# Performance work log

Hardware: AMD Instinct MI355X
Metric: run time of the kernel (lower is better)

The kernel has to match this reference:

```python
import jax, jax.numpy as jnp
import numpy as np

N_NODES = 50000
N_EDGES = 800000
D_IN = 128
D_OUT = 128


def setup_inputs() -> dict:
    key = jax.random.key(0)
    k1, k2, k3, k4, k5, k6 = jax.random.split(key, 6)
    x = jax.random.normal(k1, (N_NODES, D_IN), dtype=jnp.float32)
    edge_row = jax.random.randint(k2, (N_EDGES,), 0, N_NODES, dtype=jnp.int32)
    edge_col = jax.random.randint(k3, (N_EDGES,), 0, N_NODES, dtype=jnp.int32)
    edge_weight = jax.random.uniform(k4, (N_EDGES,), dtype=jnp.float32)
    W = jax.random.normal(k5, (D_OUT, D_IN), dtype=jnp.float32) * (1.0 / np.sqrt(D_IN))
    b = jax.random.normal(k6, (D_OUT,), dtype=jnp.float32) * 0.01
    return {"x": x, "edge_row": edge_row, "edge_col": edge_col,
            "edge_weight": edge_weight, "W": W, "b": b}


def reference(x, edge_row, edge_col, edge_weight, W, b):
    # SpMM: out[i] = sum_{e: row[e]==i} weight[e] * x[col[e]]
    msgs = edge_weight[:, None] * x[edge_col]            # [E, D_IN]
    agg = jax.ops.segment_sum(msgs, edge_row, num_segments=N_NODES)  # [N, D_IN]
    # nn.Linear: agg @ W.T + b
    return agg @ W.T + b
```

## Files before the change

### kernel.cpp

```cpp
#include <hip/hip_runtime.h>

#define D 128
#define PB 128
#define CAP 48

typedef __attribute__((ext_vector_type(8))) short bf16x8;
typedef __attribute__((ext_vector_type(4))) float f32x4;

__device__ __forceinline__ short f2bf_rne(float f) {
  unsigned u = __float_as_uint(f);
  unsigned r = u + 0x7fffu + ((u >> 16) & 1u);
  return (short)(r >> 16);
}

__device__ __forceinline__ bf16x8 pack_bf16x8(float4 a, float4 b) {
  bf16x8 h;
  h[0] = f2bf_rne(a.x); h[1] = f2bf_rne(a.y);
  h[2] = f2bf_rne(a.z); h[3] = f2bf_rne(a.w);
  h[4] = f2bf_rne(b.x); h[5] = f2bf_rne(b.y);
  h[6] = f2bf_rne(b.z); h[7] = f2bf_rne(b.w);
  return h;
}

__global__ __launch_bounds__(256) void part_gemm_kernel(
    const int* __restrict__ erow, const int* __restrict__ ecol,
    const float* __restrict__ ew, int* __restrict__ ncur,
    int2* __restrict__ swcol,
    const float* __restrict__ x, const float* __restrict__ W,
    ushort* __restrict__ y, int E, int N) {
  if (blockIdx.x < PB) {
    const int tid = threadIdx.x;
    const int chunk = (E + PB - 1) / PB;
    const int begin = blockIdx.x * chunk;
    const int end = min(begin + chunk, E);
    for (int e = begin + tid; e < end; e += 256) {
      int r = erow[e];
      int pos = atomicAdd(&ncur[r], 1);
      if (pos < CAP)
        swcol[(size_t)r * CAP + pos] =
            make_int2(ecol[e], __float_as_int(ew[e]));
    }
  } else {
    const int tid = threadIdx.x;
    const int wave = tid >> 6, lane = tid & 63;
    const int m_half = wave & 1;
    const int n_half = wave >> 1;
    const int l16 = lane & 15, quad = lane >> 4;

    bf16x8 Bf[4][4];
    const float4* W4 = (const float4*)W;
#pragma unroll
    for (int nt = 0; nt < 4; ++nt) {
      int n = n_half * 64 + nt * 16 + l16;
#pragma unroll
      for (int kb = 0; kb < 4; ++kb) {
        int idx = (n * D + kb * 32 + quad * 8) >> 2;
        Bf[nt][kb] = pack_bf16x8(W4[idx], W4[idx + 1]);
      }
    }

    const float4* x4 = (const float4*)x;
    const int ntiles = (N + 63) >> 6;
    const int gstride = gridDim.x - PB;
    for (int tile = (int)blockIdx.x - PB; tile < ntiles; tile += gstride) {
      const int row0 = tile * 64 + m_half * 32;
      f32x4 acc[2][4];
#pragma unroll
      for (int mt = 0; mt < 2; ++mt)
#pragma unroll
        for (int nt = 0; nt < 4; ++nt)
          acc[mt][nt] = (f32x4){0.f, 0.f, 0.f, 0.f};

#pragma unroll
      for (int kb = 0; kb < 4; ++kb) {
        const int k0 = kb * 32 + quad * 8;
        int m0 = row0 + l16;      if (m0 > N - 1) m0 = N - 1;
        int m1 = row0 + 16 + l16; if (m1 > N - 1) m1 = N - 1;
        int i0 = (m0 * D + k0) >> 2;
        int i1 = (m1 * D + k0) >> 2;
        float4 p0 = x4[i0], q0 = x4[i0 + 1];
        float4 p1 = x4[i1], q1 = x4[i1 + 1];
        bf16x8 a0 = pack_bf16x8(p0, q0);
        bf16x8 a1 = pack_bf16x8(p1, q1);
#pragma unroll
        for (int nt = 0; nt < 4; ++nt) {
          acc[0][nt] = __builtin_amdgcn_mfma_f32_16x16x32_bf16(a0, Bf[nt][kb], acc[0][nt], 0, 0, 0);
          acc[1][nt] = __builtin_amdgcn_mfma_f32_16x16x32_bf16(a1, Bf[nt][kb], acc[1][nt], 0, 0, 0);
        }
      }

#pragma unroll
      for (int mt = 0; mt < 2; ++mt) {
        int rbase = row0 + mt * 16 + quad * 4;
#pragma unroll
        for (int nt = 0; nt < 4; ++nt) {
          int col = n_half * 64 + nt * 16 + l16;
#pragma unroll
          for (int r = 0; r < 4; ++r) {
            int row = rbase + r;
            if (row < N) y[row * D + col] = (ushort)f2bf_rne(acc[mt][nt][r]);
          }
        }
      }
    }
  }
}

__global__ __launch_bounds__(256) void gather_agg_kernel(
    const ushort* __restrict__ y, const int* __restrict__ ncur,
    const int2* __restrict__ swcol, const float* __restrict__ bias,
    float* __restrict__ out, int N) {
  const int node = blockIdx.x * 4 + (threadIdx.x >> 6);
  const int lane = threadIdx.x & 63;
  if (node >= N) return;

  const unsigned* __restrict__ y1 = (const unsigned*)y;
  float2 acc = ((const float2*)bias)[lane];

  int cnt = ncur[node];
  if (cnt > CAP) cnt = CAP;
  const int2* __restrict__ eb = swcol + (size_t)node * CAP;
#pragma unroll 4
  for (int j = 0; j < cnt; ++j) {
    int2 cw = eb[j];
    float wg = __int_as_float(cw.y);
    unsigned v = y1[cw.x * 64 + lane];
    float f0 = __uint_as_float(v << 16);
    float f1 = __uint_as_float(v & 0xffff0000u);
    acc.x += wg * f0;
    acc.y += wg * f1;
  }
  ((float2*)out)[(size_t)node * 64 + lane] = acc;
}

extern "C" void kernel_launch(void* const* d_in, const int* in_sizes, int n_in,
                              void* d_out, int out_size, void* d_ws, size_t ws_size,
                              hipStream_t stream) {
  const float* x    = (const float*)d_in[0];
  const int*   erow = (const int*)d_in[1];
  const int*   ecol = (const int*)d_in[2];
  const float* ew   = (const float*)d_in[3];
  const float* W    = (const float*)d_in[4];
  const float* b    = (const float*)d_in[5];
  float* out = (float*)d_out;

  const int N = in_sizes[0] / D;
  const int E = in_sizes[1];

  char* ws = (char*)d_ws;
  ushort* y     = (ushort*)ws;
  int2*   swcol = (int2*)(ws + (size_t)N * D * 2);
  int*    ncur  = (int*)(swcol + (size_t)N * CAP);

  hipMemsetAsync(ncur, 0, (size_t)N * sizeof(int), stream);

  const int ntiles = (N + 63) >> 6;
  part_gemm_kernel<<<PB + ntiles, 256, 0, stream>>>(
      erow, ecol, ew, ncur, swcol, x, W, y, E, N);

  gather_agg_kernel<<<(N + 3) / 4, 256, 0, stream>>>(y, ncur, swcol, b, out, N);
}
```

Baseline: 166.5 us.

## Run partition and GEMM in every block; batch gather loads by eight

```diff
diff --git a/kernel.cpp b/kernel.cpp
--- a/kernel.cpp
+++ b/kernel.cpp
@@ -1,7 +1,7 @@
 #include <hip/hip_runtime.h>
 
 #define D 128
-#define PB 128
+#define GRID 1024
 #define CAP 48
 
 typedef __attribute__((ext_vector_type(8))) short bf16x8;
@@ -28,9 +28,10 @@
     int2* __restrict__ swcol,
     const float* __restrict__ x, const float* __restrict__ W,
     ushort* __restrict__ y, int E, int N) {
-  if (blockIdx.x < PB) {
-    const int tid = threadIdx.x;
-    const int chunk = (E + PB - 1) / PB;
+  const int tid = threadIdx.x;
+
+  {
+    const int chunk = (E + GRID - 1) / GRID;
     const int begin = blockIdx.x * chunk;
     const int end = min(begin + chunk, E);
     for (int e = begin + tid; e < end; e += 256) {
@@ -40,8 +41,9 @@
         swcol[(size_t)r * CAP + pos] =
             make_int2(ecol[e], __float_as_int(ew[e]));
     }
-  } else {
-    const int tid = threadIdx.x;
+  }
+
+  {
     const int wave = tid >> 6, lane = tid & 63;
     const int m_half = wave & 1;
     const int n_half = wave >> 1;
@@ -61,8 +63,7 @@
 
     const float4* x4 = (const float4*)x;
     const int ntiles = (N + 63) >> 6;
-    const int gstride = gridDim.x - PB;
-    for (int tile = (int)blockIdx.x - PB; tile < ntiles; tile += gstride) {
+    for (int tile = (int)blockIdx.x; tile < ntiles; tile += GRID) {
       const int row0 = tile * 64 + m_half * 32;
       f32x4 acc[2][4];
 #pragma unroll
@@ -120,15 +121,25 @@
   int cnt = ncur[node];
   if (cnt > CAP) cnt = CAP;
   const int2* __restrict__ eb = swcol + (size_t)node * CAP;
-#pragma unroll 4
-  for (int j = 0; j < cnt; ++j) {
-    int2 cw = eb[j];
-    float wg = __int_as_float(cw.y);
-    unsigned v = y1[cw.x * 64 + lane];
-    float f0 = __uint_as_float(v << 16);
-    float f1 = __uint_as_float(v & 0xffff0000u);
-    acc.x += wg * f0;
-    acc.y += wg * f1;
+
+  for (int j = 0; j < cnt; j += 8) {
+    int2 cw[8];
+#pragma unroll
+    for (int k = 0; k < 8; ++k) {
+      int idx = j + k;
+      if (idx >= cnt) idx = cnt - 1;
+      cw[k] = eb[idx];
+    }
+    unsigned v[8];
+#pragma unroll
+    for (int k = 0; k < 8; ++k)
+      v[k] = y1[cw[k].x * 64 + lane];
+#pragma unroll
+    for (int k = 0; k < 8; ++k) {
+      float wg = (j + k < cnt) ? __int_as_float(cw[k].y) : 0.0f;
+      acc.x += wg * __uint_as_float(v[k] << 16);
+      acc.y += wg * __uint_as_float(v[k] & 0xffff0000u);
+    }
   }
   ((float2*)out)[(size_t)node * 64 + lane] = acc;
 }
@@ -154,8 +165,7 @@
 
   hipMemsetAsync(ncur, 0, (size_t)N * sizeof(int), stream);
 
-  const int ntiles = (N + 63) >> 6;
-  part_gemm_kernel<<<PB + ntiles, 256, 0, stream>>>(
+  part_gemm_kernel<<<GRID, 256, 0, stream>>>(
       erow, ecol, ew, ncur, swcol, x, W, y, E, N);
 
   gather_agg_kernel<<<(N + 3) / 4, 256, 0, stream>>>(y, ncur, swcol, b, out, N);
```

Measured after the change: 189.2 us. +13.6%, slower.
